# Kernel optimization log

Measured on AMD Instinct MI355X. Metric: run time of the kernel, lower is better.

The kernel has to match this reference:

```python
import jax, jax.numpy as jnp
import numpy as np

E = 1_250_000
F = 64
N = 50_000

def setup_inputs() -> dict:
    key = jax.random.key(0)
    k1, k2 = jax.random.split(key)
    edge = jax.random.randint(k1, (2, E), 0, N, dtype=jnp.int32)
    edge_w = jax.random.normal(k2, (E, F), dtype=jnp.float32)
    return {"edge": edge, "edge_w": edge_w, "size1": N, "size2": N,
            "out_features": F, "dim": 1}

def reference(edge, edge_w, size1, size2, out_features, dim):
    # sparse_coo_tensor(edge, edge_w, [size1, size2, F]) then sparse.sum(dim)
    # == segment-sum of edge_w grouped by the surviving index row.
    # dim==1 -> group by edge[0] (output [size1, F]); dim==0 -> group by edge[1].
    if dim == 1:
        seg_ids, num_seg = edge[0], size1
    else:
        seg_ids, num_seg = edge[1], size2
    return jax.ops.segment_sum(edge_w, seg_ids, num_segments=num_seg)
```

## Files before the change

### kernel.cpp

```cpp
#include <hip/hip_runtime.h>
#include <hip/hip_bf16.h>


#define F_DIM 64

typedef __attribute__((ext_vector_type(4))) float f4v;

__global__ void zero_kernel(int* __restrict__ counts, int N) {
    const int i = blockIdx.x * blockDim.x + threadIdx.x;
    if (i < N) counts[i] = 0;
}

__global__ void rank_hist_kernel(const int* __restrict__ edge,
                                 const int* __restrict__ dim_p,
                                 int* __restrict__ counts,
                                 int* __restrict__ rank, int E) {
    const int row = (*dim_p == 1) ? 0 : 1;
    const int stride = gridDim.x * blockDim.x;
    for (int e = blockIdx.x * blockDim.x + threadIdx.x; e < E; e += stride) {
        const int seg = edge[(size_t)row * E + e];
        rank[e] = atomicAdd(&counts[seg], 1);
    }
}

__global__ void scanA_kernel(const int* __restrict__ counts,
                             int* __restrict__ offsets,
                             int* __restrict__ partials, int N) {
    __shared__ int s[256];
    const int t = threadIdx.x;
    const int idx = blockIdx.x * 256 + t;
    const int v = (idx < N) ? counts[idx] : 0;
    s[t] = v;
    __syncthreads();
    for (int d = 1; d < 256; d <<= 1) {
        const int x = (t >= d) ? s[t - d] : 0;
        __syncthreads();
        s[t] += x;
        __syncthreads();
    }
    if (idx < N) offsets[idx] = s[t] - v;
    if (t == 255) partials[blockIdx.x] = s[255];
}

__global__ void scanBC_kernel(int* __restrict__ offsets,
                              const int* __restrict__ partials,
                              int N, int E, int NB) {
    __shared__ int s[256];
    const int t = threadIdx.x;
    const int v = (t < NB) ? partials[t] : 0;
    s[t] = v;
    __syncthreads();
    for (int d = 1; d < 256; d <<= 1) {
        const int x = (t >= d) ? s[t - d] : 0;
        __syncthreads();
        s[t] += x;
        __syncthreads();
    }
    const int prefix = s[blockIdx.x] - ((blockIdx.x < NB) ? partials[blockIdx.x] : 0);
    const int idx = blockIdx.x * 256 + t;
    if (idx < N) offsets[idx] += prefix;
    if (idx == 0) offsets[N] = E;
}

__global__ void place_kernel(const int* __restrict__ edge,
                             const int* __restrict__ dim_p,
                             const int* __restrict__ offsets,
                             const int* __restrict__ rank,
                             int* __restrict__ perm, int E) {
    const int row = (*dim_p == 1) ? 0 : 1;
    const int stride = gridDim.x * blockDim.x;
    for (int e = blockIdx.x * blockDim.x + threadIdx.x; e < E; e += stride) {
        const int seg = edge[(size_t)row * E + e];
        perm[offsets[seg] + rank[e]] = e;
    }
}

__global__ __launch_bounds__(256) void gather_kernel(
    const float* __restrict__ edge_w,
    const int* __restrict__ offsets,
    const int* __restrict__ perm,
    float* __restrict__ out, int N) {
    const int node = blockIdx.x * 4 + (threadIdx.x >> 6);
    const int lane = threadIdx.x & 63;
    if (node >= N) return;
    const int beg = offsets[node];
    const int end = offsets[node + 1];
    const int grp = lane >> 3;
    const int sub = (lane & 7) << 3;
    f4v a0 = 0.0f, a1 = 0.0f;
    int j = beg + grp;
    while (j + 8 < end) {
        const int eA = perm[j];
        const int eB = perm[j + 8];
        const f4v* pA = reinterpret_cast<const f4v*>(edge_w + (size_t)eA * F_DIM + sub);
        const f4v* pB = reinterpret_cast<const f4v*>(edge_w + (size_t)eB * F_DIM + sub);
        const f4v u0 = __builtin_nontemporal_load(pA);
        const f4v u1 = __builtin_nontemporal_load(pA + 1);
        const f4v w0 = __builtin_nontemporal_load(pB);
        const f4v w1 = __builtin_nontemporal_load(pB + 1);
        a0 += u0; a1 += u1;
        a0 += w0; a1 += w1;
        j += 16;
    }
    if (j < end) {
        const int eA = perm[j];
        const f4v* pA = reinterpret_cast<const f4v*>(edge_w + (size_t)eA * F_DIM + sub);
        a0 += __builtin_nontemporal_load(pA);
        a1 += __builtin_nontemporal_load(pA + 1);
    }
    #pragma unroll
    for (int m = 8; m < 64; m <<= 1) {
        a0.x += __shfl_xor(a0.x, m); a0.y += __shfl_xor(a0.y, m);
        a0.z += __shfl_xor(a0.z, m); a0.w += __shfl_xor(a0.w, m);
        a1.x += __shfl_xor(a1.x, m); a1.y += __shfl_xor(a1.y, m);
        a1.z += __shfl_xor(a1.z, m); a1.w += __shfl_xor(a1.w, m);
    }
    if (grp == 0) {
        float* o = out + (size_t)node * F_DIM + sub;
        *reinterpret_cast<f4v*>(o)     = a0;
        *reinterpret_cast<f4v*>(o + 4) = a1;
    }
}

__global__ void atomic_kernel(const int* __restrict__ edge,
                              const float* __restrict__ edge_w,
                              const int* __restrict__ dim_p,
                              float* __restrict__ out, int E) {
    const int row = (*dim_p == 1) ? 0 : 1;
    const long long total = (long long)E * 16;
    const long long stride = (long long)gridDim.x * blockDim.x;
    for (long long i = (long long)blockIdx.x * blockDim.x + threadIdx.x;
         i < total; i += stride) {
        const int e = (int)(i >> 4);
        const int c = ((int)i & 15) << 2;
        const int seg = edge[(long long)row * E + e];
        const float4 v = *reinterpret_cast<const float4*>(
            edge_w + (long long)e * F_DIM + c);
        float* o = out + (long long)seg * F_DIM + c;
        atomicAdd(o + 0, v.x);
        atomicAdd(o + 1, v.y);
        atomicAdd(o + 2, v.z);
        atomicAdd(o + 3, v.w);
    }
}

extern "C" void kernel_launch(void* const* d_in, const int* in_sizes, int n_in,
                              void* d_out, int out_size, void* d_ws, size_t ws_size,
                              hipStream_t stream) {
    const int*   edge   = (const int*)d_in[0];
    const float* edge_w = (const float*)d_in[1];
    const int*   dim_p  = (const int*)d_in[5];
    float*       out    = (float*)d_out;

    const int E = in_sizes[0] / 2;
    const int F = in_sizes[1] / E;
    const int N = out_size / F;
    const int NB = (N + 255) / 256;

    const size_t need = ((size_t)2 * N + 1 + (size_t)E + 256) * sizeof(int);
    const bool rank_fits = (size_t)E <= (size_t)out_size;
    if (ws_size < need || NB > 256 || !rank_fits) {
        hipMemsetAsync(d_out, 0, (size_t)out_size * sizeof(float), stream);
        atomic_kernel<<<2048, 256, 0, stream>>>(edge, edge_w, dim_p, out, E);
        return;
    }

    int* counts   = (int*)d_ws;
    int* offsets  = counts + N;
    int* perm     = offsets + N + 1;
    int* partials = perm + E;
    int* rank     = (int*)d_out;

    const int block = 256;
    const int gridE = min(2048, (E + block - 1) / block);

    zero_kernel<<<NB, block, 0, stream>>>(counts, N);
    rank_hist_kernel<<<gridE, block, 0, stream>>>(edge, dim_p, counts, rank, E);
    scanA_kernel<<<NB, block, 0, stream>>>(counts, offsets, partials, N);
    scanBC_kernel<<<NB, block, 0, stream>>>(offsets, partials, N, E, NB);
    place_kernel<<<gridE, block, 0, stream>>>(edge, dim_p, offsets, rank, perm, E);

    const int gridN = (N + 3) / 4;
    gather_kernel<<<gridN, block, 0, stream>>>(edge_w, offsets, perm, out, N);
}
```

Before: 163.4 us.

## Replicate histogram counters across eight copies and vectorize edge index loads

Splits the per-segment count array into R=8 sub-histograms, chosen by edge chunk, so that fewer atomics collide on the same counter. The scan then folds the replica counts into per-replica base offsets so that placement stays deterministic and grouped by segment. Edge, rank and perm handling now use int4 vector loads with larger grids. In exchange it needs extra workspace, a larger zeroing pass, and extra gathered reads of counts8 in the place kernel.

New measurement: 160.6 us. No clear change (-1.7%).

```diff
diff --git a/kernel.cpp b/kernel.cpp
--- a/kernel.cpp
+++ b/kernel.cpp
@@ -6,31 +6,56 @@
 
 typedef __attribute__((ext_vector_type(4))) float f4v;
 
-__global__ void zero_kernel(int* __restrict__ counts, int N) {
+__global__ void zero_kernel(int* __restrict__ p, int n) {
     const int i = blockIdx.x * blockDim.x + threadIdx.x;
-    if (i < N) counts[i] = 0;
-}
-
+    if (i < n) p[i] = 0;
+}
+
+template <int R>
 __global__ void rank_hist_kernel(const int* __restrict__ edge,
                                  const int* __restrict__ dim_p,
-                                 int* __restrict__ counts,
-                                 int* __restrict__ rank, int E) {
+                                 int* __restrict__ counts8,
+                                 int* __restrict__ rank, int E, int N) {
     const int row = (*dim_p == 1) ? 0 : 1;
+    const int* er = edge + (size_t)row * E;
     const int stride = gridDim.x * blockDim.x;
-    for (int e = blockIdx.x * blockDim.x + threadIdx.x; e < E; e += stride) {
-        const int seg = edge[(size_t)row * E + e];
-        rank[e] = atomicAdd(&counts[seg], 1);
-    }
-}
-
-__global__ void scanA_kernel(const int* __restrict__ counts,
+    if ((E & 3) == 0) {
+        const int nvec = E >> 2;
+        const int4* er4 = reinterpret_cast<const int4*>(er);
+        int4* rank4 = reinterpret_cast<int4*>(rank);
+        for (int v = blockIdx.x * blockDim.x + threadIdx.x; v < nvec; v += stride) {
+            const int4 ev = er4[v];
+            const int r = (v >> 6) & (R - 1);
+            int* cb = counts8 + (size_t)r * N;
+            int4 rk;
+            rk.x = atomicAdd(&cb[ev.x], 1);
+            rk.y = atomicAdd(&cb[ev.y], 1);
+            rk.z = atomicAdd(&cb[ev.z], 1);
+            rk.w = atomicAdd(&cb[ev.w], 1);
+            rank4[v] = rk;
+        }
+    } else {
+        for (int e = blockIdx.x * blockDim.x + threadIdx.x; e < E; e += stride) {
+            const int r = (e >> 8) & (R - 1);
+            rank[e] = atomicAdd(&counts8[(size_t)r * N + er[e]], 1);
+        }
+    }
+}
+
+template <int R>
+__global__ void scanA_kernel(int* __restrict__ counts8,
                              int* __restrict__ offsets,
                              int* __restrict__ partials, int N) {
     __shared__ int s[256];
     const int t = threadIdx.x;
     const int idx = blockIdx.x * 256 + t;
-    const int v = (idx < N) ? counts[idx] : 0;
-    s[t] = v;
+    int c[R];
+    int tot = 0;
+    if (idx < N) {
+        #pragma unroll
+        for (int r = 0; r < R; ++r) { c[r] = counts8[(size_t)r * N + idx]; tot += c[r]; }
+    }
+    s[t] = tot;
     __syncthreads();
     for (int d = 1; d < 256; d <<= 1) {
         const int x = (t >= d) ? s[t - d] : 0;
@@ -38,7 +63,15 @@
         s[t] += x;
         __syncthreads();
     }
-    if (idx < N) offsets[idx] = s[t] - v;
+    if (idx < N) {
+        offsets[idx] = s[t] - tot;
+        int run = 0;
+        #pragma unroll
+        for (int r = 0; r < R; ++r) {
+            counts8[(size_t)r * N + idx] = run;
+            run += c[r];
+        }
+    }
     if (t == 255) partials[blockIdx.x] = s[255];
 }
 
@@ -62,16 +95,37 @@
     if (idx == 0) offsets[N] = E;
 }
 
+template <int R>
 __global__ void place_kernel(const int* __restrict__ edge,
                              const int* __restrict__ dim_p,
                              const int* __restrict__ offsets,
+                             const int* __restrict__ counts8,
                              const int* __restrict__ rank,
-                             int* __restrict__ perm, int E) {
+                             int* __restrict__ perm, int E, int N) {
     const int row = (*dim_p == 1) ? 0 : 1;
+    const int* er = edge + (size_t)row * E;
     const int stride = gridDim.x * blockDim.x;
-    for (int e = blockIdx.x * blockDim.x + threadIdx.x; e < E; e += stride) {
-        const int seg = edge[(size_t)row * E + e];
-        perm[offsets[seg] + rank[e]] = e;
+    if ((E & 3) == 0) {
+        const int nvec = E >> 2;
+        const int4* er4 = reinterpret_cast<const int4*>(er);
+        const int4* rank4 = reinterpret_cast<const int4*>(rank);
+        for (int v = blockIdx.x * blockDim.x + threadIdx.x; v < nvec; v += stride) {
+            const int4 ev = er4[v];
+            const int4 rk = rank4[v];
+            const int r = (v >> 6) & (R - 1);
+            const int* cb = counts8 + (size_t)r * N;
+            const int e = v << 2;
+            perm[offsets[ev.x] + cb[ev.x] + rk.x] = e + 0;
+            perm[offsets[ev.y] + cb[ev.y] + rk.y] = e + 1;
+            perm[offsets[ev.z] + cb[ev.z] + rk.z] = e + 2;
+            perm[offsets[ev.w] + cb[ev.w] + rk.w] = e + 3;
+        }
+    } else {
+        for (int e = blockIdx.x * blockDim.x + threadIdx.x; e < E; e += stride) {
+            const int r = (e >> 8) & (R - 1);
+            const int seg = er[e];
+            perm[offsets[seg] + counts8[(size_t)r * N + seg] + rank[e]] = e;
+        }
     }
 }
 
@@ -157,28 +211,43 @@
     const int N = out_size / F;
     const int NB = (N + 255) / 256;
 
-    const size_t need = ((size_t)2 * N + 1 + (size_t)E + 256) * sizeof(int);
+    const size_t need8 = ((size_t)8 * N + N + 1 + (size_t)E + 256) * sizeof(int);
+    const size_t need1 = ((size_t)1 * N + N + 1 + (size_t)E + 256) * sizeof(int);
     const bool rank_fits = (size_t)E <= (size_t)out_size;
-    if (ws_size < need || NB > 256 || !rank_fits) {
+    if (ws_size < need1 || NB > 256 || !rank_fits) {
         hipMemsetAsync(d_out, 0, (size_t)out_size * sizeof(float), stream);
         atomic_kernel<<<2048, 256, 0, stream>>>(edge, edge_w, dim_p, out, E);
         return;
     }
-
-    int* counts   = (int*)d_ws;
-    int* offsets  = counts + N;
+    const int R = (ws_size >= need8) ? 8 : 1;
+
+    int* counts8  = (int*)d_ws;
+    int* offsets  = counts8 + (size_t)R * N;
     int* perm     = offsets + N + 1;
     int* partials = perm + E;
     int* rank     = (int*)d_out;
 
     const int block = 256;
-    const int gridE = min(2048, (E + block - 1) / block);
-
-    zero_kernel<<<NB, block, 0, stream>>>(counts, N);
-    rank_hist_kernel<<<gridE, block, 0, stream>>>(edge, dim_p, counts, rank, E);
-    scanA_kernel<<<NB, block, 0, stream>>>(counts, offsets, partials, N);
-    scanBC_kernel<<<NB, block, 0, stream>>>(offsets, partials, N, E, NB);
-    place_kernel<<<gridE, block, 0, stream>>>(edge, dim_p, offsets, rank, perm, E);
+    const int gridV = min(4096, (E / 4 + block - 1) / block);
+    const int gridE = min(4096, (E + block - 1) / block);
+    const int gridZ = (R * N + block - 1) / block;
+
+    zero_kernel<<<gridZ, block, 0, stream>>>(counts8, R * N);
+    if (R == 8) {
+        rank_hist_kernel<8><<<(E & 3) ? gridE : gridV, block, 0, stream>>>(
+            edge, dim_p, counts8, rank, E, N);
+        scanA_kernel<8><<<NB, block, 0, stream>>>(counts8, offsets, partials, N);
+        scanBC_kernel<<<NB, block, 0, stream>>>(offsets, partials, N, E, NB);
+        place_kernel<8><<<(E & 3) ? gridE : gridV, block, 0, stream>>>(
+            edge, dim_p, offsets, counts8, rank, perm, E, N);
+    } else {
+        rank_hist_kernel<1><<<(E & 3) ? gridE : gridV, block, 0, stream>>>(
+            edge, dim_p, counts8, rank, E, N);
+        scanA_kernel<1><<<NB, block, 0, stream>>>(counts8, offsets, partials, N);
+        scanBC_kernel<<<NB, block, 0, stream>>>(offsets, partials, N, E, NB);
+        place_kernel<1><<<(E & 3) ? gridE : gridV, block, 0, stream>>>(
+            edge, dim_p, offsets, counts8, rank, perm, E, N);
+    }
 
     const int gridN = (N + 3) / 4;
     gather_kernel<<<gridN, block, 0, stream>>>(edge_w, offsets, perm, out, N);
```
